# Optimization experiments

Measured on AMD Instinct MI355X. Metric: run time of the kernel, lower is better.

## Reference

```python
import jax, jax.numpy as jnp
import numpy as np

TAU = 1.0
REDUCTION = 'mean'


def setup_inputs() -> dict:
    key = jax.random.key(0)
    k1, k2 = jax.random.split(key)
    n, d, n_classes = 8192, 128, 100
    projection = jax.random.normal(k1, (n, d), dtype=jnp.float32)
    y = jax.random.randint(k2, (n,), 0, n_classes, dtype=jnp.int64)
    return {"projection": projection, "y": y}


def reference(projection, y):
    n = projection.shape[0]
    sim = projection @ projection.T  # [n, n]
    eq = y[:, None] == y[None, :]
    same_mask = eq & ~jnp.eye(n, dtype=bool)  # same class, excluding self
    diff_mask = ~eq

    big = jnp.asarray(jnp.inf, dtype=sim.dtype)
    # masked per-row min over same-class sims (0 if row has none)
    min_same = jnp.min(jnp.where(same_mask, sim, big), axis=1)
    min_same = jnp.where(jnp.any(same_mask, axis=1), min_same, 0.0)
    # masked per-row max over diff-class sims (0 if row has none)
    max_diff = jnp.max(jnp.where(diff_mask, sim, -big), axis=1)
    max_diff = jnp.where(jnp.any(diff_mask, axis=1), max_diff, 0.0)

    loss_i = jnp.maximum(0.0, min_same + max_diff + TAU)  # [n]
    if REDUCTION == 'mean':
        return jnp.mean(loss_i)
    return jnp.sum(loss_i)
```

## Files before the change

kernel.cpp:

```cpp
#include <hip/hip_runtime.h>
#include <hip/hip_bf16.h>
#include <float.h>

#define N 8192
#define D 128
#define BM 256
#define BN 64
#define GY 16
#define COLS_PER_BLOCK (N / GY)
#define TILES (COLS_PER_BLOCK / BN)
#define NPART GY
#define LOSS_BLOCKS (N / 256)

typedef unsigned short u16;
typedef unsigned int u32;
typedef __attribute__((ext_vector_type(8))) short bf16x8;
typedef __attribute__((ext_vector_type(4))) float f32x4;

typedef const __attribute__((address_space(1))) u32 glb_u32;
typedef __attribute__((address_space(3))) u32 lds_u32;

__device__ inline u16 f32_to_bf16_rtne(float f) {
  union { float f; unsigned int u; } c; c.f = f;
  unsigned int u = c.u;
  u += 0x7FFFu + ((u >> 16) & 1u);
  return (u16)(u >> 16);
}

__global__ __launch_bounds__(256) void convert_kernel(const float* __restrict__ P,
                                                      u16* __restrict__ Pb) {
  int i = blockIdx.x * 256 + threadIdx.x;
  float4 v = reinterpret_cast<const float4*>(P)[i];
  uint2 o;
  o.x = (unsigned)f32_to_bf16_rtne(v.x) | ((unsigned)f32_to_bf16_rtne(v.y) << 16);
  o.y = (unsigned)f32_to_bf16_rtne(v.z) | ((unsigned)f32_to_bf16_rtne(v.w) << 16);
  reinterpret_cast<uint2*>(Pb)[i] = o;
}

template <bool DIAG>
__device__ __forceinline__ void pipeline(const char* __restrict__ pbb,
                                         const int* __restrict__ y,
                                         float* __restrict__ pmin,
                                         float* __restrict__ pmax,
                                         char* ldsB, int* ldsY,
                                         int R0, int C0, int slot) {
  const int tid  = threadIdx.x;
  const int w    = tid >> 6;
  const int lane = tid & 63;
  const int c15  = lane & 15;
  const int g    = lane >> 4;

  {
    const int* gy = y + C0 + w * 128 + lane;
    lds_u32* dst = (lds_u32*)(ldsY + w * 128);
    __builtin_amdgcn_global_load_lds((glb_u32*)gy,        dst,      4, 0, 0);
    __builtin_amdgcn_global_load_lds((glb_u32*)(gy + 64), dst + 64, 4, 0, 0);
  }

  auto STAGE = [&](int buf, int t) {
    const char* gb = pbb + (size_t)(C0 + t * BN) * 256;
    char* base = ldsB + buf * (BN * 256);
#pragma unroll
    for (int j = 0; j < 4; ++j) {
      const int L = ((w * 4 + j) * 64 + lane) * 16;
      const int c = L >> 8;
      const int o = L & 255;
      const int src = c * 256 + (o ^ ((c & 15) << 4));
      __builtin_amdgcn_global_load_lds((glb_u32*)(gb + src),
                                       (lds_u32*)(base + (w * 4 + j) * 1024), 16, 0, 0);
    }
  };

  STAGE(0, 0);
  STAGE(1, 1);

  bf16x8 afrag[4][4];
#pragma unroll
  for (int rg = 0; rg < 4; ++rg) {
    const char* ap = pbb + (size_t)(R0 + w * 64 + rg * 16 + c15) * 256 + g * 16;
#pragma unroll
    for (int kk = 0; kk < 4; ++kk)
      afrag[rg][kk] = *reinterpret_cast<const bf16x8*>(ap + kk * 64);
  }

  int rowI[4][4], yrow[4][4];
#pragma unroll
  for (int rg = 0; rg < 4; ++rg)
#pragma unroll
    for (int r = 0; r < 4; ++r) {
      rowI[rg][r] = R0 + w * 64 + rg * 16 + g * 4 + r;
      yrow[rg][r] = y[rowI[rg][r]];
    }

  float mins[4][4], maxd[4][4];
#pragma unroll
  for (int rg = 0; rg < 4; ++rg)
#pragma unroll
    for (int r = 0; r < 4; ++r) { mins[rg][r] = FLT_MAX; maxd[rg][r] = -FLT_MAX; }

#pragma unroll 1
  for (int t = 0; t < TILES; ++t) {
    if (t + 1 < TILES) asm volatile("s_waitcnt vmcnt(4)" ::: "memory");
    else               asm volatile("s_waitcnt vmcnt(0)" ::: "memory");
    __builtin_amdgcn_s_barrier();
    if (t + 2 < TILES) STAGE((t + 2) % 3, t + 2);

    const char* Bb = ldsB + (t % 3) * (BN * 256);
    const int ct0 = t * BN;
#pragma unroll
    for (int s = 0; s < 4; ++s) {
      const int c = s * 16 + c15;
      bf16x8 bf[4];
#pragma unroll
      for (int kk = 0; kk < 4; ++kk) {
        const int off = c * 256 + (((g * 16) | (kk * 64)) ^ (c15 << 4));
        bf[kk] = *reinterpret_cast<const bf16x8*>(Bb + off);
      }
      f32x4 acc[4];
#pragma unroll
      for (int rg = 0; rg < 4; ++rg) acc[rg] = (f32x4){0.f, 0.f, 0.f, 0.f};
#pragma unroll
      for (int kk = 0; kk < 4; ++kk)
#pragma unroll
        for (int rg = 0; rg < 4; ++rg)
          acc[rg] = __builtin_amdgcn_mfma_f32_16x16x32_bf16(afrag[rg][kk], bf[kk],
                                                            acc[rg], 0, 0, 0);
      const int colB = ct0 + c;
      const int col  = C0 + colB;
      const int ycol = ldsY[colB];
#pragma unroll
      for (int rg = 0; rg < 4; ++rg)
#pragma unroll
        for (int r = 0; r < 4; ++r) {
          const float v = acc[rg][r];
          const bool same = (ycol == yrow[rg][r]);
          bool okmin = same;
          if (DIAG) okmin = same && (col != rowI[rg][r]);
          const float cmin = okmin ? v : FLT_MAX;
          const float cmax = same ? -FLT_MAX : v;
          mins[rg][r] = fminf(mins[rg][r], cmin);
          maxd[rg][r] = fmaxf(maxd[rg][r], cmax);
        }
    }
  }

#pragma unroll
  for (int off = 1; off < 16; off <<= 1)
#pragma unroll
    for (int rg = 0; rg < 4; ++rg)
#pragma unroll
      for (int r = 0; r < 4; ++r) {
        mins[rg][r] = fminf(mins[rg][r], __shfl_xor(mins[rg][r], off, 64));
        maxd[rg][r] = fmaxf(maxd[rg][r], __shfl_xor(maxd[rg][r], off, 64));
      }

  if (c15 == 0) {
#pragma unroll
    for (int rg = 0; rg < 4; ++rg)
#pragma unroll
      for (int r = 0; r < 4; ++r) {
        pmin[(size_t)slot * N + rowI[rg][r]] = mins[rg][r];
        pmax[(size_t)slot * N + rowI[rg][r]] = maxd[rg][r];
      }
  }
}

__global__ __launch_bounds__(256, 2) void margin_main(const u16* __restrict__ Pb,
                                                      const int* __restrict__ y,
                                                      float* __restrict__ pmin,
                                                      float* __restrict__ pmax) {
  __shared__ __align__(16) char ldsB[3][BN * 256];
  __shared__ int ldsY[COLS_PER_BLOCK];
  const int R0 = blockIdx.x * BM;
  const int C0 = blockIdx.y * COLS_PER_BLOCK;
  if ((unsigned)(R0 - C0) < (unsigned)COLS_PER_BLOCK)
    pipeline<true>((const char*)Pb, y, pmin, pmax, &ldsB[0][0], ldsY, R0, C0, blockIdx.y);
  else
    pipeline<false>((const char*)Pb, y, pmin, pmax, &ldsB[0][0], ldsY, R0, C0, blockIdx.y);
}

__global__ __launch_bounds__(256) void loss_kernel(const float* __restrict__ pmin,
                                                   const float* __restrict__ pmax,
                                                   float* __restrict__ blockSums) {
  const int row = blockIdx.x * 256 + threadIdx.x;
  float mn = FLT_MAX, mx = -FLT_MAX;
#pragma unroll
  for (int s = 0; s < NPART; ++s) {
    mn = fminf(mn, pmin[(size_t)s * N + row]);
    mx = fmaxf(mx, pmax[(size_t)s * N + row]);
  }
  if (mn == FLT_MAX)  mn = 0.f;
  if (mx == -FLT_MAX) mx = 0.f;
  float loss = fmaxf(0.f, mn + mx + 1.0f);

#pragma unroll
  for (int off = 32; off >= 1; off >>= 1)
    loss += __shfl_down(loss, off, 64);
  __shared__ float wsum[4];
  if ((threadIdx.x & 63) == 0) wsum[threadIdx.x >> 6] = loss;
  __syncthreads();
  if (threadIdx.x == 0)
    blockSums[blockIdx.x] = wsum[0] + wsum[1] + wsum[2] + wsum[3];
}

__global__ __launch_bounds__(64) void finalize_kernel(const float* __restrict__ blockSums,
                                                      float* __restrict__ out) {
  float v = (threadIdx.x < LOSS_BLOCKS) ? blockSums[threadIdx.x] : 0.f;
#pragma unroll
  for (int off = 32; off >= 1; off >>= 1)
    v += __shfl_down(v, off, 64);
  if (threadIdx.x == 0) out[0] = v / (float)N;
}

extern "C" void kernel_launch(void* const* d_in, const int* in_sizes, int n_in,
                              void* d_out, int out_size, void* d_ws, size_t ws_size,
                              hipStream_t stream) {
  const float* P = (const float*)d_in[0];
  const int*   y = (const int*)d_in[1];
  float* out = (float*)d_out;

  u16*   Pb        = (u16*)d_ws;
  float* pmin      = (float*)((char*)d_ws + (size_t)N * D * sizeof(u16));
  float* pmax      = pmin + (size_t)N * NPART;
  float* blockSums = pmax + (size_t)N * NPART;

  convert_kernel<<<dim3(N * D / 4 / 256), 256, 0, stream>>>(P, Pb);
  margin_main<<<dim3(N / BM, GY), 256, 0, stream>>>(Pb, y, pmin, pmax);
  loss_kernel<<<dim3(LOSS_BLOCKS), 256, 0, stream>>>(pmin, pmax, blockSums);
  finalize_kernel<<<1, 64, 0, stream>>>(blockSums, out);
}
```

Baseline: 38.56 us.

## Split row tile across eight waves per block and raise MFMA priority

Doubles the waves per block from 4 to 8, so each wave now handles 32 rows instead of 64. This halves the per-wave A fragments, accumulators and min/max state, and the staging loads are spread over more waves. Launch bounds change to 512 threads with a requested 4 blocks per CU to raise occupancy and latency hiding. s_setprio is placed around the MFMA chain. In exchange, each B fragment read from LDS now feeds half as many MFMAs, which doubles LDS read traffic per FLOP.

```diff
diff --git a/kernel.cpp b/kernel.cpp
--- a/kernel.cpp
+++ b/kernel.cpp
@@ -4,6 +4,7 @@
 
 #define N 8192
 #define D 128
+#define WAVES 8
 #define BM 256
 #define BN 64
 #define GY 16
@@ -50,63 +51,58 @@
   const int c15  = lane & 15;
   const int g    = lane >> 4;
 
-  {
-    const int* gy = y + C0 + w * 128 + lane;
-    lds_u32* dst = (lds_u32*)(ldsY + w * 128);
-    __builtin_amdgcn_global_load_lds((glb_u32*)gy,        dst,      4, 0, 0);
-    __builtin_amdgcn_global_load_lds((glb_u32*)(gy + 64), dst + 64, 4, 0, 0);
-  }
+  __builtin_amdgcn_global_load_lds((glb_u32*)(y + C0 + w * 64 + lane),
+                                   (lds_u32*)(ldsY + w * 64), 4, 0, 0);
 
   auto STAGE = [&](int buf, int t) {
     const char* gb = pbb + (size_t)(C0 + t * BN) * 256;
     char* base = ldsB + buf * (BN * 256);
 #pragma unroll
-    for (int j = 0; j < 4; ++j) {
-      const int L = ((w * 4 + j) * 64 + lane) * 16;
+    for (int j = 0; j < 2; ++j) {
+      const int L = ((w * 2 + j) * 64 + lane) * 16;
       const int c = L >> 8;
       const int o = L & 255;
       const int src = c * 256 + (o ^ ((c & 15) << 4));
       __builtin_amdgcn_global_load_lds((glb_u32*)(gb + src),
-                                       (lds_u32*)(base + (w * 4 + j) * 1024), 16, 0, 0);
+                                       (lds_u32*)(base + (w * 2 + j) * 1024), 16, 0, 0);
     }
   };
 
   STAGE(0, 0);
   STAGE(1, 1);
 
-  bf16x8 afrag[4][4];
-#pragma unroll
-  for (int rg = 0; rg < 4; ++rg) {
-    const char* ap = pbb + (size_t)(R0 + w * 64 + rg * 16 + c15) * 256 + g * 16;
+  const int rowbase = R0 + w * 32 + g * 4;
+
+  bf16x8 afrag[2][4];
+#pragma unroll
+  for (int rg = 0; rg < 2; ++rg) {
+    const char* ap = pbb + (size_t)(R0 + w * 32 + rg * 16 + c15) * 256 + g * 16;
 #pragma unroll
     for (int kk = 0; kk < 4; ++kk)
       afrag[rg][kk] = *reinterpret_cast<const bf16x8*>(ap + kk * 64);
   }
 
-  int rowI[4][4], yrow[4][4];
-#pragma unroll
-  for (int rg = 0; rg < 4; ++rg)
-#pragma unroll
-    for (int r = 0; r < 4; ++r) {
-      rowI[rg][r] = R0 + w * 64 + rg * 16 + g * 4 + r;
-      yrow[rg][r] = y[rowI[rg][r]];
-    }
-
-  float mins[4][4], maxd[4][4];
-#pragma unroll
-  for (int rg = 0; rg < 4; ++rg)
+  int yrow[2][4];
+#pragma unroll
+  for (int rg = 0; rg < 2; ++rg)
+#pragma unroll
+    for (int r = 0; r < 4; ++r)
+      yrow[rg][r] = y[rowbase + rg * 16 + r];
+
+  float mins[2][4], maxd[2][4];
+#pragma unroll
+  for (int rg = 0; rg < 2; ++rg)
 #pragma unroll
     for (int r = 0; r < 4; ++r) { mins[rg][r] = FLT_MAX; maxd[rg][r] = -FLT_MAX; }
 
 #pragma unroll 1
   for (int t = 0; t < TILES; ++t) {
-    if (t + 1 < TILES) asm volatile("s_waitcnt vmcnt(4)" ::: "memory");
+    if (t + 1 < TILES) asm volatile("s_waitcnt vmcnt(2)" ::: "memory");
     else               asm volatile("s_waitcnt vmcnt(0)" ::: "memory");
     __builtin_amdgcn_s_barrier();
     if (t + 2 < TILES) STAGE((t + 2) % 3, t + 2);
 
     const char* Bb = ldsB + (t % 3) * (BN * 256);
-    const int ct0 = t * BN;
 #pragma unroll
     for (int s = 0; s < 4; ++s) {
       const int c = s * 16 + c15;
@@ -116,38 +112,43 @@
         const int off = c * 256 + (((g * 16) | (kk * 64)) ^ (c15 << 4));
         bf[kk] = *reinterpret_cast<const bf16x8*>(Bb + off);
       }
-      f32x4 acc[4];
-#pragma unroll
-      for (int rg = 0; rg < 4; ++rg) acc[rg] = (f32x4){0.f, 0.f, 0.f, 0.f};
-#pragma unroll
-      for (int kk = 0; kk < 4; ++kk)
-#pragma unroll
-        for (int rg = 0; rg < 4; ++rg)
-          acc[rg] = __builtin_amdgcn_mfma_f32_16x16x32_bf16(afrag[rg][kk], bf[kk],
-                                                            acc[rg], 0, 0, 0);
-      const int colB = ct0 + c;
+      f32x4 acc0 = {0.f, 0.f, 0.f, 0.f}, acc1 = {0.f, 0.f, 0.f, 0.f};
+      __builtin_amdgcn_s_setprio(1);
+#pragma unroll
+      for (int kk = 0; kk < 4; ++kk) {
+        acc0 = __builtin_amdgcn_mfma_f32_16x16x32_bf16(afrag[0][kk], bf[kk], acc0, 0, 0, 0);
+        acc1 = __builtin_amdgcn_mfma_f32_16x16x32_bf16(afrag[1][kk], bf[kk], acc1, 0, 0, 0);
+      }
+      __builtin_amdgcn_s_setprio(0);
+      const int colB = t * BN + c;
+      const int ycol = ldsY[colB];
       const int col  = C0 + colB;
-      const int ycol = ldsY[colB];
-#pragma unroll
-      for (int rg = 0; rg < 4; ++rg)
-#pragma unroll
-        for (int r = 0; r < 4; ++r) {
-          const float v = acc[rg][r];
-          const bool same = (ycol == yrow[rg][r]);
+#pragma unroll
+      for (int r = 0; r < 4; ++r) {
+        {
+          const float v = acc0[r];
+          const bool same = (ycol == yrow[0][r]);
           bool okmin = same;
-          if (DIAG) okmin = same && (col != rowI[rg][r]);
-          const float cmin = okmin ? v : FLT_MAX;
-          const float cmax = same ? -FLT_MAX : v;
-          mins[rg][r] = fminf(mins[rg][r], cmin);
-          maxd[rg][r] = fmaxf(maxd[rg][r], cmax);
+          if (DIAG) okmin = same && (col != rowbase + r);
+          mins[0][r] = fminf(mins[0][r], okmin ? v : FLT_MAX);
+          maxd[0][r] = fmaxf(maxd[0][r], same ? -FLT_MAX : v);
         }
+        {
+          const float v = acc1[r];
+          const bool same = (ycol == yrow[1][r]);
+          bool okmin = same;
+          if (DIAG) okmin = same && (col != rowbase + 16 + r);
+          mins[1][r] = fminf(mins[1][r], okmin ? v : FLT_MAX);
+          maxd[1][r] = fmaxf(maxd[1][r], same ? -FLT_MAX : v);
+        }
+      }
     }
   }
 
 #pragma unroll
   for (int off = 1; off < 16; off <<= 1)
 #pragma unroll
-    for (int rg = 0; rg < 4; ++rg)
+    for (int rg = 0; rg < 2; ++rg)
 #pragma unroll
       for (int r = 0; r < 4; ++r) {
         mins[rg][r] = fminf(mins[rg][r], __shfl_xor(mins[rg][r], off, 64));
@@ -156,16 +157,16 @@
 
   if (c15 == 0) {
 #pragma unroll
-    for (int rg = 0; rg < 4; ++rg)
+    for (int rg = 0; rg < 2; ++rg)
 #pragma unroll
       for (int r = 0; r < 4; ++r) {
-        pmin[(size_t)slot * N + rowI[rg][r]] = mins[rg][r];
-        pmax[(size_t)slot * N + rowI[rg][r]] = maxd[rg][r];
-      }
-  }
-}
-
-__global__ __launch_bounds__(256, 2) void margin_main(const u16* __restrict__ Pb,
+        pmin[(size_t)slot * N + rowbase + rg * 16 + r] = mins[rg][r];
+        pmax[(size_t)slot * N + rowbase + rg * 16 + r] = maxd[rg][r];
+      }
+  }
+}
+
+__global__ __launch_bounds__(512, 4) void margin_main(const u16* __restrict__ Pb,
                                                       const int* __restrict__ y,
                                                       float* __restrict__ pmin,
                                                       float* __restrict__ pmax) {
@@ -225,7 +226,7 @@
   float* blockSums = pmax + (size_t)N * NPART;
 
   convert_kernel<<<dim3(N * D / 4 / 256), 256, 0, stream>>>(P, Pb);
-  margin_main<<<dim3(N / BM, GY), 256, 0, stream>>>(Pb, y, pmin, pmax);
+  margin_main<<<dim3(N / BM, GY), 512, 0, stream>>>(Pb, y, pmin, pmax);
   loss_kernel<<<dim3(LOSS_BLOCKS), 256, 0, stream>>>(pmin, pmax, blockSums);
   finalize_kernel<<<1, 64, 0, stream>>>(blockSums, out);
 }
```

New measurement: 39.55 us. +2.6%, slower.

## Sort rows by class so most tiles skip same-class masking

Applied to the files above, without the earlier changes.

Adds a counting-sort kernel that groups rows by label and a gather kernel that converts the permuted rows to bf16. In the main kernel each wave computes the column range of its classes, and 16-column subtiles outside that range take a cheap max-only path without label compares. It also raises wave priority around the MFMA block. This adds an extra kernel launch plus a per-class scan over the labels, and it assumes exactly 100 classes with labels in [0,100).

```diff
diff --git a/kernel.cpp b/kernel.cpp
--- a/kernel.cpp
+++ b/kernel.cpp
@@ -4,6 +4,7 @@
 
 #define N 8192
 #define D 128
+#define NCLS 100
 #define BM 256
 #define BN 64
 #define GY 16
@@ -20,38 +21,104 @@
 typedef const __attribute__((address_space(1))) u32 glb_u32;
 typedef __attribute__((address_space(3))) u32 lds_u32;
 
-__device__ inline u16 f32_to_bf16_rtne(float f) {
-  union { float f; unsigned int u; } c; c.f = f;
-  unsigned int u = c.u;
-  u += 0x7FFFu + ((u >> 16) & 1u);
-  return (u16)(u >> 16);
-}
-
-__global__ __launch_bounds__(256) void convert_kernel(const float* __restrict__ P,
-                                                      u16* __restrict__ Pb) {
-  int i = blockIdx.x * 256 + threadIdx.x;
-  float4 v = reinterpret_cast<const float4*>(P)[i];
-  uint2 o;
-  o.x = (unsigned)f32_to_bf16_rtne(v.x) | ((unsigned)f32_to_bf16_rtne(v.y) << 16);
-  o.y = (unsigned)f32_to_bf16_rtne(v.z) | ((unsigned)f32_to_bf16_rtne(v.w) << 16);
-  reinterpret_cast<uint2*>(Pb)[i] = o;
-}
-
-template <bool DIAG>
-__device__ __forceinline__ void pipeline(const char* __restrict__ pbb,
-                                         const int* __restrict__ y,
-                                         float* __restrict__ pmin,
-                                         float* __restrict__ pmax,
-                                         char* ldsB, int* ldsY,
-                                         int R0, int C0, int slot) {
+__device__ __forceinline__ u32 pack_bf16x2(float a, float b) {
+  u32 ua = __float_as_uint(a); ua += 0x7FFFu + ((ua >> 16) & 1u);
+  u32 ub = __float_as_uint(b); ub += 0x7FFFu + ((ub >> 16) & 1u);
+  return (ua >> 16) | (ub & 0xFFFF0000u);
+}
+
+__global__ __launch_bounds__(256) void sort_kernel(const int* __restrict__ y,
+                                                   int* __restrict__ perm,
+                                                   int* __restrict__ yp,
+                                                   int* __restrict__ rs,
+                                                   int* __restrict__ re) {
+  const int c    = blockIdx.x;
+  const int ww   = threadIdx.x >> 6;
+  const int lane = threadIdx.x & 63;
+  const int base0 = ww * (N / 4);
+
+  int lt = 0, eq = 0;
+#pragma unroll 2
+  for (int i = 0; i < N / 4; i += 256) {
+    int v0 = y[base0 + i + lane];
+    int v1 = y[base0 + i + 64 + lane];
+    int v2 = y[base0 + i + 128 + lane];
+    int v3 = y[base0 + i + 192 + lane];
+    lt += (v0 < c) + (v1 < c) + (v2 < c) + (v3 < c);
+    eq += (v0 == c) + (v1 == c) + (v2 == c) + (v3 == c);
+  }
+#pragma unroll
+  for (int off = 32; off >= 1; off >>= 1) {
+    lt += __shfl_down(lt, off, 64);
+    eq += __shfl_down(eq, off, 64);
+  }
+  __shared__ int ltW[4], eqW[4];
+  if (lane == 0) { ltW[ww] = lt; eqW[ww] = eq; }
+  __syncthreads();
+  const int start = ltW[0] + ltW[1] + ltW[2] + ltW[3];
+  const int cnt   = eqW[0] + eqW[1] + eqW[2] + eqW[3];
+  const int end   = start + cnt;
+  int run = start;
+  for (int w2 = 0; w2 < ww; ++w2) run += eqW[w2];
+
+  const unsigned long long below = (lane == 0) ? 0ull : ((1ull << lane) - 1ull);
+#pragma unroll 2
+  for (int i = 0; i < N / 4; i += 128) {
+    int v0 = y[base0 + i + lane];
+    int v1 = y[base0 + i + 64 + lane];
+    unsigned long long m0 = __ballot(v0 == c);
+    unsigned long long m1 = __ballot(v1 == c);
+    if (v0 == c) {
+      int pos = run + __popcll(m0 & below);
+      perm[pos] = base0 + i + lane; yp[pos] = c; rs[pos] = start; re[pos] = end;
+    }
+    run += __popcll(m0);
+    if (v1 == c) {
+      int pos = run + __popcll(m1 & below);
+      perm[pos] = base0 + i + 64 + lane; yp[pos] = c; rs[pos] = start; re[pos] = end;
+    }
+    run += __popcll(m1);
+  }
+}
+
+__global__ __launch_bounds__(256) void gather_kernel(const float* __restrict__ P,
+                                                     const int* __restrict__ perm,
+                                                     u16* __restrict__ Pp) {
+  const int rloc = threadIdx.x >> 4;
+  const int t16  = threadIdx.x & 15;
+  const int k    = blockIdx.x * 16 + rloc;
+  const int src  = perm[k];
+  const float4* s = reinterpret_cast<const float4*>(P + (size_t)src * D) + t16 * 2;
+  float4 v0 = s[0], v1 = s[1];
+  uint4 o;
+  o.x = pack_bf16x2(v0.x, v0.y);
+  o.y = pack_bf16x2(v0.z, v0.w);
+  o.z = pack_bf16x2(v1.x, v1.y);
+  o.w = pack_bf16x2(v1.z, v1.w);
+  reinterpret_cast<uint4*>(Pp + (size_t)k * D)[t16] = o;
+}
+
+__global__ __launch_bounds__(256) void margin_main(const u16* __restrict__ Pp,
+                                                   const int* __restrict__ yp,
+                                                   const int* __restrict__ rs,
+                                                   const int* __restrict__ re,
+                                                   float* __restrict__ pmin,
+                                                   float* __restrict__ pmax) {
+  __shared__ __align__(16) char ldsB[3][BN * 256];
+  __shared__ int ldsY[COLS_PER_BLOCK];
+
   const int tid  = threadIdx.x;
   const int w    = tid >> 6;
   const int lane = tid & 63;
   const int c15  = lane & 15;
   const int g    = lane >> 4;
 
+  const int R0 = blockIdx.x * BM;
+  const int C0 = blockIdx.y * COLS_PER_BLOCK;
+  const char* pbb = (const char*)Pp;
+
   {
-    const int* gy = y + C0 + w * 128 + lane;
+    const int* gy = yp + C0 + w * 128 + lane;
     lds_u32* dst = (lds_u32*)(ldsY + w * 128);
     __builtin_amdgcn_global_load_lds((glb_u32*)gy,        dst,      4, 0, 0);
     __builtin_amdgcn_global_load_lds((glb_u32*)(gy + 64), dst + 64, 4, 0, 0);
@@ -59,12 +126,11 @@
 
   auto STAGE = [&](int buf, int t) {
     const char* gb = pbb + (size_t)(C0 + t * BN) * 256;
-    char* base = ldsB + buf * (BN * 256);
+    char* base = &ldsB[buf][0];
 #pragma unroll
     for (int j = 0; j < 4; ++j) {
       const int L = ((w * 4 + j) * 64 + lane) * 16;
-      const int c = L >> 8;
-      const int o = L & 255;
+      const int c = L >> 8, o = L & 255;
       const int src = c * 256 + (o ^ ((c & 15) << 4));
       __builtin_amdgcn_global_load_lds((glb_u32*)(gb + src),
                                        (lds_u32*)(base + (w * 4 + j) * 1024), 16, 0, 0);
@@ -74,29 +140,30 @@
   STAGE(0, 0);
   STAGE(1, 1);
 
+  const int R0w = R0 + w * 64;
+  const int stripLo = __builtin_amdgcn_readfirstlane(rs[R0w]);
+  const int stripHi = __builtin_amdgcn_readfirstlane(re[R0w + 63]);
+
   bf16x8 afrag[4][4];
 #pragma unroll
   for (int rg = 0; rg < 4; ++rg) {
-    const char* ap = pbb + (size_t)(R0 + w * 64 + rg * 16 + c15) * 256 + g * 16;
+    const char* ap = pbb + (size_t)(R0w + rg * 16 + c15) * 256 + g * 16;
 #pragma unroll
     for (int kk = 0; kk < 4; ++kk)
       afrag[rg][kk] = *reinterpret_cast<const bf16x8*>(ap + kk * 64);
   }
-
-  int rowI[4][4], yrow[4][4];
+  int yrow[4][4];
 #pragma unroll
   for (int rg = 0; rg < 4; ++rg)
 #pragma unroll
-    for (int r = 0; r < 4; ++r) {
-      rowI[rg][r] = R0 + w * 64 + rg * 16 + g * 4 + r;
-      yrow[rg][r] = y[rowI[rg][r]];
-    }
-
-  float mins[4][4], maxd[4][4];
+    for (int r = 0; r < 4; ++r)
+      yrow[rg][r] = yp[R0w + rg * 16 + g * 4 + r];
+
+  float rmin[4][4], rmax[4][4];
 #pragma unroll
   for (int rg = 0; rg < 4; ++rg)
 #pragma unroll
-    for (int r = 0; r < 4; ++r) { mins[rg][r] = FLT_MAX; maxd[rg][r] = -FLT_MAX; }
+    for (int r = 0; r < 4; ++r) { rmin[rg][r] = FLT_MAX; rmax[rg][r] = -FLT_MAX; }
 
 #pragma unroll 1
   for (int t = 0; t < TILES; ++t) {
@@ -105,8 +172,7 @@
     __builtin_amdgcn_s_barrier();
     if (t + 2 < TILES) STAGE((t + 2) % 3, t + 2);
 
-    const char* Bb = ldsB + (t % 3) * (BN * 256);
-    const int ct0 = t * BN;
+    const char* Bb = &ldsB[t % 3][0];
 #pragma unroll
     for (int s = 0; s < 4; ++s) {
       const int c = s * 16 + c15;
@@ -119,28 +185,36 @@
       f32x4 acc[4];
 #pragma unroll
       for (int rg = 0; rg < 4; ++rg) acc[rg] = (f32x4){0.f, 0.f, 0.f, 0.f};
+      __builtin_amdgcn_s_setprio(1);
 #pragma unroll
       for (int kk = 0; kk < 4; ++kk)
 #pragma unroll
         for (int rg = 0; rg < 4; ++rg)
           acc[rg] = __builtin_amdgcn_mfma_f32_16x16x32_bf16(afrag[rg][kk], bf[kk],
                                                             acc[rg], 0, 0, 0);
-      const int colB = ct0 + c;
-      const int col  = C0 + colB;
-      const int ycol = ldsY[colB];
-#pragma unroll
-      for (int rg = 0; rg < 4; ++rg)
-#pragma unroll
-        for (int r = 0; r < 4; ++r) {
-          const float v = acc[rg][r];
-          const bool same = (ycol == yrow[rg][r]);
-          bool okmin = same;
-          if (DIAG) okmin = same && (col != rowI[rg][r]);
-          const float cmin = okmin ? v : FLT_MAX;
-          const float cmax = same ? -FLT_MAX : v;
-          mins[rg][r] = fminf(mins[rg][r], cmin);
-          maxd[rg][r] = fmaxf(maxd[rg][r], cmax);
-        }
+      __builtin_amdgcn_s_setprio(0);
+
+      const int colT = C0 + t * BN + s * 16;
+      if (colT + 16 <= stripLo || colT >= stripHi) {
+#pragma unroll
+        for (int rg = 0; rg < 4; ++rg)
+#pragma unroll
+          for (int r = 0; r < 4; ++r)
+            rmax[rg][r] = fmaxf(rmax[rg][r], acc[rg][r]);
+      } else {
+        const int ycol = ldsY[t * BN + s * 16 + c15];
+        const int colg = colT + c15;
+#pragma unroll
+        for (int rg = 0; rg < 4; ++rg)
+#pragma unroll
+          for (int r = 0; r < 4; ++r) {
+            const float v = acc[rg][r];
+            const bool same = (ycol == yrow[rg][r]);
+            const bool okmin = same && (colg != R0w + rg * 16 + g * 4 + r);
+            rmin[rg][r] = fminf(rmin[rg][r], okmin ? v : FLT_MAX);
+            rmax[rg][r] = fmaxf(rmax[rg][r], same ? -FLT_MAX : v);
+          }
+      }
     }
   }
 
@@ -150,8 +224,8 @@
     for (int rg = 0; rg < 4; ++rg)
 #pragma unroll
       for (int r = 0; r < 4; ++r) {
-        mins[rg][r] = fminf(mins[rg][r], __shfl_xor(mins[rg][r], off, 64));
-        maxd[rg][r] = fmaxf(maxd[rg][r], __shfl_xor(maxd[rg][r], off, 64));
+        rmin[rg][r] = fminf(rmin[rg][r], __shfl_xor(rmin[rg][r], off, 64));
+        rmax[rg][r] = fmaxf(rmax[rg][r], __shfl_xor(rmax[rg][r], off, 64));
       }
 
   if (c15 == 0) {
@@ -159,24 +233,11 @@
     for (int rg = 0; rg < 4; ++rg)
 #pragma unroll
       for (int r = 0; r < 4; ++r) {
-        pmin[(size_t)slot * N + rowI[rg][r]] = mins[rg][r];
-        pmax[(size_t)slot * N + rowI[rg][r]] = maxd[rg][r];
-      }
-  }
-}
-
-__global__ __launch_bounds__(256, 2) void margin_main(const u16* __restrict__ Pb,
-                                                      const int* __restrict__ y,
-                                                      float* __restrict__ pmin,
-                                                      float* __restrict__ pmax) {
-  __shared__ __align__(16) char ldsB[3][BN * 256];
-  __shared__ int ldsY[COLS_PER_BLOCK];
-  const int R0 = blockIdx.x * BM;
-  const int C0 = blockIdx.y * COLS_PER_BLOCK;
-  if ((unsigned)(R0 - C0) < (unsigned)COLS_PER_BLOCK)
-    pipeline<true>((const char*)Pb, y, pmin, pmax, &ldsB[0][0], ldsY, R0, C0, blockIdx.y);
-  else
-    pipeline<false>((const char*)Pb, y, pmin, pmax, &ldsB[0][0], ldsY, R0, C0, blockIdx.y);
+        const int row = R0w + rg * 16 + g * 4 + r;
+        pmin[(size_t)blockIdx.y * N + row] = rmin[rg][r];
+        pmax[(size_t)blockIdx.y * N + row] = rmax[rg][r];
+      }
+  }
 }
 
 __global__ __launch_bounds__(256) void loss_kernel(const float* __restrict__ pmin,
@@ -219,13 +280,18 @@
   const int*   y = (const int*)d_in[1];
   float* out = (float*)d_out;
 
-  u16*   Pb        = (u16*)d_ws;
-  float* pmin      = (float*)((char*)d_ws + (size_t)N * D * sizeof(u16));
-  float* pmax      = pmin + (size_t)N * NPART;
+  u16* Pp   = (u16*)d_ws;
+  int* perm = (int*)((char*)d_ws + (size_t)N * D * sizeof(u16));
+  int* yp   = perm + N;
+  int* rs   = yp + N;
+  int* re   = rs + N;
+  float* pmin = (float*)(re + N);
+  float* pmax = pmin + (size_t)N * NPART;
   float* blockSums = pmax + (size_t)N * NPART;
 
-  convert_kernel<<<dim3(N * D / 4 / 256), 256, 0, stream>>>(P, Pb);
-  margin_main<<<dim3(N / BM, GY), 256, 0, stream>>>(Pb, y, pmin, pmax);
+  sort_kernel<<<dim3(NCLS), 256, 0, stream>>>(y, perm, yp, rs, re);
+  gather_kernel<<<dim3(N / 16), 256, 0, stream>>>(P, perm, Pp);
+  margin_main<<<dim3(N / BM, GY), 256, 0, stream>>>(Pp, yp, rs, re, pmin, pmax);
   loss_kernel<<<dim3(LOSS_BLOCKS), 256, 0, stream>>>(pmin, pmax, blockSums);
   finalize_kernel<<<1, 64, 0, stream>>>(blockSums, out);
 }
```

Measured after the change: 46.50 us. 20.6% more time.
